# Optimization experiments

Hardware: AMD Instinct MI355X
Metric: run time of the kernel (lower is better)

Reference implementation:

```python
import jax, jax.numpy as jnp
import numpy as np


def setup_inputs() -> dict:
    key = jax.random.key(0)
    k1, k2, k3 = jax.random.split(key, 3)
    B, T, D = 64, 256, 512
    real = jax.random.normal(k1, (B, T, D), dtype=jnp.float32)
    imag = jax.random.normal(k2, (B, T, D), dtype=jnp.float32)
    weight = jax.random.uniform(k3, (B, T, 1), dtype=jnp.float32)
    return {"real": real, "imag": imag, "weight": weight}


def reference(real, imag, weight):
    # Weighted complex outer-product mixture:
    #   out_r[b] = sum_t w[b,t] * (r_t r_t^T + i_t i_t^T)
    #   out_i[b] = sum_t w[b,t] * (i_t r_t^T - r_t i_t^T)
    # Equivalent to the original per-sample loop + TxDxD outer products,
    # but fused: scale one operand by w and contract over t directly.
    w = weight[..., 0]  # [B, T]
    rw = real * w[..., None]  # [B, T, D]
    iw = imag * w[..., None]
    out_r = jnp.einsum('btd,bte->bde', rw, real) + jnp.einsum('btd,bte->bde', iw, imag)
    out_i = jnp.einsum('btd,bte->bde', iw, real) - jnp.einsum('btd,bte->bde', rw, imag)
    return (out_r, out_i)
```

## Files before the change

### kernel.cpp

```cpp
#include <hip/hip_runtime.h>
#include <cstdint>
#include <cstddef>

#define BB 64
#define TT 256
#define DD 512
#define BK 32
#define TILEM 128

typedef short bf16x8 __attribute__((ext_vector_type(8)));
typedef float f32x4  __attribute__((ext_vector_type(4)));
typedef int   i32x4  __attribute__((ext_vector_type(4)));

static __device__ __forceinline__ unsigned short f2bf(float x) {
  unsigned u = __builtin_bit_cast(unsigned, x) + 0x8000u;
  return (unsigned short)(u >> 16);
}

__global__ __launch_bounds__(256, 2)
void ComplexMixture_54838142435828_kernel(const float* __restrict__ re,
                                          const float* __restrict__ im,
                                          const float* __restrict__ wt,
                                          float* __restrict__ out) {
  __shared__ __attribute__((aligned(16))) char smem[33792];
  unsigned short* sAr = (unsigned short*)(smem);
  unsigned short* sAi = (unsigned short*)(smem + 8192);
  unsigned short* sBr = (unsigned short*)(smem + 16384);
  unsigned short* sBi = (unsigned short*)(smem + 24576);
  float*          sw  = (float*)(smem + 32768);

  const int tid = threadIdx.x;

  const int L = blockIdx.x;
  const int c = L & 7;
  const int s = L >> 3;
  const int b  = c * 8 + s / 10;
  const int t  = s % 10;
  const int ti = (t >= 6) ? 3 : (t >= 3) ? 2 : (t >= 1) ? 1 : 0;
  const int tj = t - ((ti * (ti + 1)) >> 1);
  const int d0 = ti * TILEM;
  const int e0 = tj * TILEM;

  sw[tid] = wt[b * TT + tid];

  const int lane = tid & 63;
  const int wid  = tid >> 6;
  const int wm = (wid >> 1) * 64;
  const int wn = (wid & 1) * 64;
  const int quad = lane >> 4;
  const int l16  = lane & 15;

  const int q     = tid & 31;
  const int h     = (tid >> 5) & 1;
  const int warr  = (tid >> 6) & 1;
  const int wside = tid >> 7;
  unsigned short* dst = wside ? (warr ? sBi : sBr) : (warr ? sAi : sAr);
  const float* srcArr = warr ? im : re;
  const int panel = wside ? e0 : d0;
  const int swm = (q >> 1) & 3;

  const int l16b = l16 ^ ((l16 >> 3) & 1);

  f32x4 accR[4][4], accI[4][4];
  #pragma unroll
  for (int mt = 0; mt < 4; ++mt)
    #pragma unroll
    for (int nt = 0; nt < 4; ++nt) {
      accR[mt][nt] = (f32x4){0.f, 0.f, 0.f, 0.f};
      accI[mt][nt] = (f32x4){0.f, 0.f, 0.f, 0.f};
    }

  for (int kt = 0; kt < TT; kt += BK) {
    __syncthreads();

    const int kb = kt + h * 16;
    const float* rowPtr = srcArr + ((size_t)(b * TT + kb)) * DD + panel + q * 4;
    f32x4 v[16];
    #pragma unroll
    for (int k = 0; k < 16; ++k)
      v[k] = *(const f32x4*)(rowPtr + (size_t)k * DD);
    if (!wside) {
      #pragma unroll
      for (int k = 0; k < 16; ++k)
        v[k] *= sw[kb + k];
    }
    #pragma unroll
    for (int oc = 0; oc < 2; ++oc) {
      #pragma unroll
      for (int dd = 0; dd < 4; ++dd) {
        union { unsigned short hh[8]; i32x4 qq; } u;
        #pragma unroll
        for (int j = 0; j < 8; ++j)
          u.hh[j] = f2bf(v[oc * 8 + j][dd]);
        const int g = ((2 * h + oc) * 128 + 4 * q + (dd ^ swm));
        *(i32x4*)&dst[g * 8] = u.qq;
      }
    }
    __syncthreads();

    bf16x8 aR[4], aI[4], bR[4], bI[4];
    #pragma unroll
    for (int tt = 0; tt < 4; ++tt) {
      const int rsw = l16b ^ ((tt & 1) << 1);
      const int ga = (quad * 128 + wm + tt * 16 + rsw) * 8;
      const int gb = (quad * 128 + wn + tt * 16 + rsw) * 8;
      aR[tt] = *(const bf16x8*)&sAr[ga];
      aI[tt] = *(const bf16x8*)&sAi[ga];
      bR[tt] = *(const bf16x8*)&sBr[gb];
      bI[tt] = *(const bf16x8*)&sBi[gb];
    }
    #pragma unroll
    for (int mt = 0; mt < 4; ++mt) {
      const bf16x8 aRn = aR[mt] ^ (bf16x8)((short)0x8000);
      #pragma unroll
      for (int nt = 0; nt < 4; ++nt) {
        accR[mt][nt] = __builtin_amdgcn_mfma_f32_16x16x32_bf16(aR[mt], bR[nt], accR[mt][nt], 0, 0, 0);
        accR[mt][nt] = __builtin_amdgcn_mfma_f32_16x16x32_bf16(aI[mt], bI[nt], accR[mt][nt], 0, 0, 0);
        accI[mt][nt] = __builtin_amdgcn_mfma_f32_16x16x32_bf16(aI[mt], bR[nt], accI[mt][nt], 0, 0, 0);
        accI[mt][nt] = __builtin_amdgcn_mfma_f32_16x16x32_bf16(aRn,    bI[nt], accI[mt][nt], 0, 0, 0);
      }
    }
  }

  __syncthreads();

  const size_t NOFF = (size_t)BB * DD * DD;
  #pragma unroll
  for (int mt = 0; mt < 4; ++mt) {
    #pragma unroll
    for (int r = 0; r < 4; ++r) {
      const int drow = d0 + wm + mt * 16 + quad * 4 + r;
      const size_t rowOff = ((size_t)(b * DD + drow)) * DD;
      #pragma unroll
      for (int nt = 0; nt < 4; ++nt) {
        const int ecol = e0 + wn + nt * 16 + l16;
        out[rowOff + ecol]        = accR[mt][nt][r];
        out[NOFF + rowOff + ecol] = accI[mt][nt][r];
      }
    }
  }

  if (ti != tj) {
    float* tbR = (float*)(smem + wid * 8192);
    float* tbI = tbR + 1024;
    #pragma unroll
    for (int mt = 0; mt < 4; ++mt) {
      #pragma unroll
      for (int nt = 0; nt < 4; ++nt) {
        #pragma unroll
        for (int r = 0; r < 4; ++r) {
          const int a = (quad * 4 + r) * 64 + nt * 16 + l16;
          tbR[a] = accR[mt][nt][r];
          tbI[a] = -accI[mt][nt][r];
        }
      }
      const size_t trOff = ((size_t)(b * DD + e0 + wn + lane)) * DD
                         + (size_t)(d0 + wm + mt * 16);
      #pragma unroll
      for (int j = 0; j < 4; ++j) {
        f32x4 vr, vi;
        #pragma unroll
        for (int qq = 0; qq < 4; ++qq) {
          vr[qq] = tbR[(j * 4 + qq) * 64 + lane];
          vi[qq] = tbI[(j * 4 + qq) * 64 + lane];
        }
        *(f32x4*)&out[trOff + j * 4]        = vr;
        *(f32x4*)&out[NOFF + trOff + j * 4] = vi;
      }
    }
  }
}

extern "C" void kernel_launch(void* const* d_in, const int* in_sizes, int n_in,
                              void* d_out, int out_size, void* d_ws, size_t ws_size,
                              hipStream_t stream) {
  const float* re = (const float*)d_in[0];
  const float* im = (const float*)d_in[1];
  const float* wt = (const float*)d_in[2];
  float* out = (float*)d_out;
  ComplexMixture_54838142435828_kernel<<<dim3(640), dim3(256), 0, stream>>>(re, im, wt, out);
}
```

Baseline: 211.8 us.

## Double-buffer LDS tiles with 512-thread blocks and coalesced transposed epilogue

Doubles the block to 512 threads (8 waves, each computing 64x32 of the 128x128 tile) and double-buffers the bf16 LDS tiles. Global loads for the next K-step are issued before the MFMAs of the current step and written to the other buffer afterward, so each iteration needs only one barrier. Weights are read directly as vectors from global memory instead of being staged in LDS. The epilogue now stages accumulators through swizzled LDS so both the direct and the mirrored (transposed) output tiles are written as 16-byte vector stores. The cost is 64 KB of LDS per block, which may limit occupancy, plus more register pressure from the prefetched values.

```diff
diff --git a/kernel.cpp b/kernel.cpp
--- a/kernel.cpp
+++ b/kernel.cpp
@@ -7,6 +7,7 @@
 #define DD 512
 #define BK 32
 #define TILEM 128
+#define NITER (TT / BK)
 
 typedef short bf16x8 __attribute__((ext_vector_type(8)));
 typedef float f32x4  __attribute__((ext_vector_type(4)));
@@ -17,17 +18,12 @@
   return (unsigned short)(u >> 16);
 }
 
-__global__ __launch_bounds__(256, 2)
+__global__ __launch_bounds__(512, 2)
 void ComplexMixture_54838142435828_kernel(const float* __restrict__ re,
                                           const float* __restrict__ im,
                                           const float* __restrict__ wt,
                                           float* __restrict__ out) {
-  __shared__ __attribute__((aligned(16))) char smem[33792];
-  unsigned short* sAr = (unsigned short*)(smem);
-  unsigned short* sAi = (unsigned short*)(smem + 8192);
-  unsigned short* sBr = (unsigned short*)(smem + 16384);
-  unsigned short* sBi = (unsigned short*)(smem + 24576);
-  float*          sw  = (float*)(smem + 32768);
+  __shared__ __attribute__((aligned(16))) char smem[65536];
 
   const int tid = threadIdx.x;
 
@@ -41,132 +37,182 @@
   const int d0 = ti * TILEM;
   const int e0 = tj * TILEM;
 
-  sw[tid] = wt[b * TT + tid];
-
   const int lane = tid & 63;
   const int wid  = tid >> 6;
-  const int wm = (wid >> 1) * 64;
-  const int wn = (wid & 1) * 64;
+  const int wm   = (wid >> 2) * 64;
+  const int wn   = (wid & 3) * 32;
   const int quad = lane >> 4;
   const int l16  = lane & 15;
 
-  const int q     = tid & 31;
-  const int h     = (tid >> 5) & 1;
-  const int warr  = (tid >> 6) & 1;
-  const int wside = tid >> 7;
-  unsigned short* dst = wside ? (warr ? sBi : sBr) : (warr ? sAi : sAr);
-  const float* srcArr = warr ? im : re;
-  const int panel = wside ? e0 : d0;
-  const int swm = (q >> 1) & 3;
-
-  const int l16b = l16 ^ ((l16 >> 3) & 1);
-
-  f32x4 accR[4][4], accI[4][4];
+  const int g  = tid >> 7;
+  const int tq = tid & 31;
+  const int th = (tid >> 5) & 3;
+  const bool aside = (g < 2);
+  const float* src = (g & 1) ? im : re;
+  const int panel  = aside ? d0 : e0;
+  const int subOff = g * 8192;
+
+  int wgo[4];
+  #pragma unroll
+  for (int dd = 0; dd < 4; ++dd)
+    wgo[dd] = (th * 128 + 4 * tq + (dd ^ (tq & 3) ^ ((tq >> 2) & 1))) * 16;
+
+  const size_t colBase = (size_t)(b * TT) * DD + panel + tq * 4;
+  const float* wtb = wt + b * TT;
+
+  f32x4 accR[4][2], accI[4][2];
   #pragma unroll
   for (int mt = 0; mt < 4; ++mt)
     #pragma unroll
-    for (int nt = 0; nt < 4; ++nt) {
+    for (int nt = 0; nt < 2; ++nt) {
       accR[mt][nt] = (f32x4){0.f, 0.f, 0.f, 0.f};
       accI[mt][nt] = (f32x4){0.f, 0.f, 0.f, 0.f};
     }
 
-  for (int kt = 0; kt < TT; kt += BK) {
-    __syncthreads();
-
-    const int kb = kt + h * 16;
-    const float* rowPtr = srcArr + ((size_t)(b * TT + kb)) * DD + panel + q * 4;
-    f32x4 v[16];
-    #pragma unroll
-    for (int k = 0; k < 16; ++k)
-      v[k] = *(const f32x4*)(rowPtr + (size_t)k * DD);
-    if (!wside) {
-      #pragma unroll
-      for (int k = 0; k < 16; ++k)
-        v[k] *= sw[kb + k];
-    }
-    #pragma unroll
-    for (int oc = 0; oc < 2; ++oc) {
-      #pragma unroll
-      for (int dd = 0; dd < 4; ++dd) {
-        union { unsigned short hh[8]; i32x4 qq; } u;
-        #pragma unroll
-        for (int j = 0; j < 8; ++j)
-          u.hh[j] = f2bf(v[oc * 8 + j][dd]);
-        const int g = ((2 * h + oc) * 128 + 4 * q + (dd ^ swm));
-        *(i32x4*)&dst[g * 8] = u.qq;
-      }
-    }
-    __syncthreads();
-
-    bf16x8 aR[4], aI[4], bR[4], bI[4];
-    #pragma unroll
-    for (int tt = 0; tt < 4; ++tt) {
-      const int rsw = l16b ^ ((tt & 1) << 1);
-      const int ga = (quad * 128 + wm + tt * 16 + rsw) * 8;
-      const int gb = (quad * 128 + wn + tt * 16 + rsw) * 8;
-      aR[tt] = *(const bf16x8*)&sAr[ga];
-      aI[tt] = *(const bf16x8*)&sAi[ga];
-      bR[tt] = *(const bf16x8*)&sBr[gb];
-      bI[tt] = *(const bf16x8*)&sBi[gb];
-    }
+  f32x4 v[8];
+  f32x4 w0 = (f32x4){1.f,1.f,1.f,1.f}, w1 = w0;
+
+  #pragma unroll
+  for (int k = 0; k < 8; ++k)
+    v[k] = *(const f32x4*)(src + colBase + (size_t)(th * 8 + k) * DD);
+  if (aside) {
+    w0 = *(const f32x4*)(wtb + th * 8);
+    w1 = *(const f32x4*)(wtb + th * 8 + 4);
+  }
+  {
+    char* wb = smem + subOff;
+    if (aside) {
+      #pragma unroll
+      for (int k = 0; k < 4; ++k) v[k] *= w0[k];
+      #pragma unroll
+      for (int k = 0; k < 4; ++k) v[k + 4] *= w1[k];
+    }
+    #pragma unroll
+    for (int dd = 0; dd < 4; ++dd) {
+      union { unsigned short hh[8]; i32x4 q; } u;
+      #pragma unroll
+      for (int j = 0; j < 8; ++j) u.hh[j] = f2bf(v[j][dd]);
+      *(i32x4*)(wb + wgo[dd]) = u.q;
+    }
+  }
+
+  #pragma unroll
+  for (int it = 0; it < NITER; ++it) {
+    const int ktn = it * BK + BK;
+    const int rbo = (it & 1) * 32768;
+
+    if (ktn < TT) {
+      #pragma unroll
+      for (int k = 0; k < 8; ++k)
+        v[k] = *(const f32x4*)(src + colBase + (size_t)(ktn + th * 8 + k) * DD);
+      if (aside) {
+        w0 = *(const f32x4*)(wtb + ktn + th * 8);
+        w1 = *(const f32x4*)(wtb + ktn + th * 8 + 4);
+      }
+    }
+
+    asm volatile("s_waitcnt lgkmcnt(0)\n\ts_barrier" ::: "memory");
+
+    const char* rb = smem + rbo;
+    bf16x8 aR[4], aI[4], bR[2], bI[2];
+    #pragma unroll
+    for (int mt = 0; mt < 4; ++mt) {
+      const int r  = wm + mt * 16 + l16;
+      const int gi = (quad * 128 + (r & ~3) +
+                      ((r & 3) ^ ((r >> 2) & 3) ^ ((r >> 4) & 1))) * 16;
+      aR[mt] = *(const bf16x8*)(rb + gi);
+      aI[mt] = *(const bf16x8*)(rb + 8192 + gi);
+    }
+    #pragma unroll
+    for (int nt = 0; nt < 2; ++nt) {
+      const int r  = wn + nt * 16 + l16;
+      const int gi = (quad * 128 + (r & ~3) +
+                      ((r & 3) ^ ((r >> 2) & 3) ^ ((r >> 4) & 1))) * 16;
+      bR[nt] = *(const bf16x8*)(rb + 16384 + gi);
+      bI[nt] = *(const bf16x8*)(rb + 24576 + gi);
+    }
+
     #pragma unroll
     for (int mt = 0; mt < 4; ++mt) {
       const bf16x8 aRn = aR[mt] ^ (bf16x8)((short)0x8000);
       #pragma unroll
-      for (int nt = 0; nt < 4; ++nt) {
+      for (int nt = 0; nt < 2; ++nt) {
         accR[mt][nt] = __builtin_amdgcn_mfma_f32_16x16x32_bf16(aR[mt], bR[nt], accR[mt][nt], 0, 0, 0);
         accR[mt][nt] = __builtin_amdgcn_mfma_f32_16x16x32_bf16(aI[mt], bI[nt], accR[mt][nt], 0, 0, 0);
         accI[mt][nt] = __builtin_amdgcn_mfma_f32_16x16x32_bf16(aI[mt], bR[nt], accI[mt][nt], 0, 0, 0);
         accI[mt][nt] = __builtin_amdgcn_mfma_f32_16x16x32_bf16(aRn,    bI[nt], accI[mt][nt], 0, 0, 0);
       }
     }
-  }
-
-  __syncthreads();
+
+    if (ktn < TT) {
+      char* wb = smem + ((it & 1) ^ 1) * 32768 + subOff;
+      if (aside) {
+        #pragma unroll
+        for (int k = 0; k < 4; ++k) v[k] *= w0[k];
+        #pragma unroll
+        for (int k = 0; k < 4; ++k) v[k + 4] *= w1[k];
+      }
+      #pragma unroll
+      for (int dd = 0; dd < 4; ++dd) {
+        union { unsigned short hh[8]; i32x4 q; } u;
+        #pragma unroll
+        for (int j = 0; j < 8; ++j) u.hh[j] = f2bf(v[j][dd]);
+        *(i32x4*)(wb + wgo[dd]) = u.q;
+      }
+    }
+  }
 
   const size_t NOFF = (size_t)BB * DD * DD;
+  float* tbR = (float*)(smem + wid * 4096);
+  float* tbI = tbR + 512;
+  const bool offdiag = (ti != tj);
+
   #pragma unroll
   for (int mt = 0; mt < 4; ++mt) {
     #pragma unroll
-    for (int r = 0; r < 4; ++r) {
-      const int drow = d0 + wm + mt * 16 + quad * 4 + r;
-      const size_t rowOff = ((size_t)(b * DD + drow)) * DD;
-      #pragma unroll
-      for (int nt = 0; nt < 4; ++nt) {
-        const int ecol = e0 + wn + nt * 16 + l16;
-        out[rowOff + ecol]        = accR[mt][nt][r];
-        out[NOFF + rowOff + ecol] = accI[mt][nt][r];
-      }
-    }
-  }
-
-  if (ti != tj) {
-    float* tbR = (float*)(smem + wid * 8192);
-    float* tbI = tbR + 1024;
-    #pragma unroll
-    for (int mt = 0; mt < 4; ++mt) {
-      #pragma unroll
-      for (int nt = 0; nt < 4; ++nt) {
-        #pragma unroll
-        for (int r = 0; r < 4; ++r) {
-          const int a = (quad * 4 + r) * 64 + nt * 16 + l16;
-          tbR[a] = accR[mt][nt][r];
-          tbI[a] = -accI[mt][nt][r];
-        }
-      }
-      const size_t trOff = ((size_t)(b * DD + e0 + wn + lane)) * DD
-                         + (size_t)(d0 + wm + mt * 16);
-      #pragma unroll
-      for (int j = 0; j < 4; ++j) {
-        f32x4 vr, vi;
-        #pragma unroll
-        for (int qq = 0; qq < 4; ++qq) {
-          vr[qq] = tbR[(j * 4 + qq) * 64 + lane];
-          vi[qq] = tbI[(j * 4 + qq) * 64 + lane];
-        }
-        *(f32x4*)&out[trOff + j * 4]        = vr;
-        *(f32x4*)&out[NOFF + trOff + j * 4] = vi;
-      }
+    for (int nt = 0; nt < 2; ++nt)
+      #pragma unroll
+      for (int r = 0; r < 4; ++r) {
+        const int a = (quad * 4 + r) * 32 + ((nt * 16 + l16) ^ (quad << 3));
+        tbR[a] = accR[mt][nt][r];
+        tbI[a] = accI[mt][nt][r];
+      }
+    {
+      const int rowD = lane >> 2;
+      const int ech  = (lane & 3) * 8;
+      const int a0   = rowD * 32 + (ech ^ ((rowD >> 2) << 3));
+      const f32x4 r0 = *(const f32x4*)&tbR[a0];
+      const f32x4 r1 = *(const f32x4*)&tbR[a0 + 4];
+      const f32x4 i0 = *(const f32x4*)&tbI[a0];
+      const f32x4 i1 = *(const f32x4*)&tbI[a0 + 4];
+      const size_t ro = ((size_t)(b * DD + d0 + wm + mt * 16 + rowD)) * DD
+                      + (size_t)(e0 + wn + ech);
+      *(f32x4*)&out[ro]            = r0;
+      *(f32x4*)&out[ro + 4]        = r1;
+      *(f32x4*)&out[NOFF + ro]     = i0;
+      *(f32x4*)&out[NOFF + ro + 4] = i1;
+    }
+    if (offdiag) {
+      const int er = lane & 31;
+      const int hf = lane >> 5;
+      f32x4 rr0, rr1, ii0, ii1;
+      #pragma unroll
+      for (int j2 = 0; j2 < 4; ++j2) {
+        const int p0 = hf * 8 + j2;
+        const int p1 = hf * 8 + 4 + j2;
+        const int a0 = p0 * 32 + (er ^ ((p0 >> 2) << 3));
+        const int a1 = p1 * 32 + (er ^ ((p1 >> 2) << 3));
+        rr0[j2] =  tbR[a0];
+        rr1[j2] =  tbR[a1];
+        ii0[j2] = -tbI[a0];
+        ii1[j2] = -tbI[a1];
+      }
+      const size_t mo = ((size_t)(b * DD + e0 + wn + er)) * DD
+                      + (size_t)(d0 + wm + mt * 16 + hf * 8);
+      *(f32x4*)&out[mo]            = rr0;
+      *(f32x4*)&out[mo + 4]        = rr1;
+      *(f32x4*)&out[NOFF + mo]     = ii0;
+      *(f32x4*)&out[NOFF + mo + 4] = ii1;
     }
   }
 }
@@ -178,5 +224,5 @@
   const float* im = (const float*)d_in[1];
   const float* wt = (const float*)d_in[2];
   float* out = (float*)d_out;
-  ComplexMixture_54838142435828_kernel<<<dim3(640), dim3(256), 0, stream>>>(re, im, wt, out);
+  ComplexMixture_54838142435828_kernel<<<dim3(640), dim3(512), 0, stream>>>(re, im, wt, out);
 }
```

Result: faster. 207.5 us (-2.0%).
